# Kernel tuning notes

Hardware: AMD Instinct MI355X
Metric: run time of the kernel (lower is better)

The kernel has to match this reference:

```python
import jax, jax.numpy as jnp
import numpy as np

N_NODES = 20000
N_EDGES = 640000
FEAT = 128


def setup_inputs() -> dict:
    key = jax.random.key(0)
    k1, k2, k3, k4 = jax.random.split(key, 4)
    x = jax.random.normal(k1, (1, N_NODES, FEAT, 4), dtype=jnp.float32)
    edge_index = jax.random.randint(k2, (2, N_EDGES), 0, N_NODES, dtype=jnp.int64)
    # Linear(in_channels=128, out_channels=128): W [out, in], b [out]
    W = jax.random.normal(k3, (FEAT, FEAT), dtype=jnp.float32) * 0.05
    b = jax.random.normal(k4, (FEAT,), dtype=jnp.float32) * 0.05
    return {"x": x, "edge_index": edge_index, "W": W, "b": b}


def reference(x, edge_index, W, b):
    # x: [B, N, F, T]
    B, N, F, T = x.shape
    # permute -> [B, T, N, F]; Linear over feature dim (out == in == F)
    h = jnp.einsum('bnft,of->btno', x, W) + b          # [B, T, N, F]
    h = h.reshape(B * T, N, F)                          # flatten batch*time
    src = edge_index[0]  # message source (x_j)
    dst = edge_index[1]  # scatter target
    msgs = h[:, src, :]                                 # [B*T, E, F] gather
    # scatter-max per target node (PyG aggr='max'); vmap over batch*time
    agg = jax.vmap(lambda m: jax.ops.segment_max(m, dst, num_segments=N))(msgs)
    # nodes with no incoming edges: segment_max yields -inf -> 0 (PyG fill)
    agg = jnp.where(jnp.isneginf(agg), jnp.zeros_like(agg), agg)
    out = agg.reshape(B, T, N, F).transpose(0, 2, 3, 1)  # [B, N, F, T]
    return out
```

## Files before the change

### kernel.cpp

```cpp
#include <hip/hip_runtime.h>
#include <hip/hip_bf16.h>
#include <stdint.h>

#define N_NODES 20000
#define N_EDGES 640000
#define FEAT 128
#define CAPD 128
#define NPHASE 8

typedef __attribute__((ext_vector_type(8))) short bf16x8;
typedef __attribute__((ext_vector_type(4))) float f32x4;

__device__ __forceinline__ unsigned pkbf16(float lo, float hi) {
  __hip_bfloat162 p = __float22bfloat162_rn(make_float2(lo, hi));
  return *reinterpret_cast<unsigned*>(&p);
}

__device__ __forceinline__ unsigned short enc16(float f) {
  unsigned a = __float_as_uint(f);
  unsigned b = (a + 0x7FFFu + ((a >> 16) & 1u)) >> 16;
  unsigned s = (unsigned)((int)a >> 31);
  return (unsigned short)((b ^ 0x8000u) ^ (s & 0x7FFFu));
}

__device__ __forceinline__ float dec16(unsigned e) {
  unsigned b = (e & 0x8000u) ? (e ^ 0x8000u) : (e ^ 0xFFFFu);
  return __uint_as_float(b << 16);
}

__device__ __forceinline__ void pmax(unsigned& a, unsigned v) {
  asm("v_pk_max_u16 %0, %0, %1" : "+v"(a) : "v"(v));
}

#define PMX4(v)                                              \
  do {                                                       \
    pmax(a0, (v).x); pmax(a1, (v).y);                        \
    pmax(a2, (v).z); pmax(a3, (v).w);                        \
  } while (0)

__global__ __launch_bounds__(256) void scatter_kernel(const int* __restrict__ ei,
                                                      int* __restrict__ cnt,
                                                      unsigned short* __restrict__ csr,
                                                      const float* __restrict__ W,
                                                      unsigned short* __restrict__ Wbf) {
  int t = blockIdx.x * 256 + threadIdx.x;
  if (t < FEAT * FEAT / 2) {
    float2 w = ((const float2*)W)[t];
    ((unsigned*)Wbf)[t] = pkbf16(w.x, w.y);
  }
  int src = ei[t];
  int dst = ei[N_EDGES + t];
  int pos = atomicAdd(&cnt[dst], 1);
  if (pos < CAPD) csr[(size_t)dst * CAPD + pos] = (unsigned short)src;
}

__global__ __launch_bounds__(256) void gemm_kernel(
    const float4* __restrict__ x, const unsigned short* __restrict__ Wbf,
    const float* __restrict__ b, uint4* __restrict__ h) {
  __shared__ __align__(16) unsigned short sm[17408 / 2];
  const int tid = threadIdx.x;
  const int n0 = blockIdx.x * 16;

#pragma unroll
  for (int it = 0; it < 4; ++it) {
    int e = tid + it * 256;
    int n = e >> 6, fp = e & 63;
    float4 a = x[(size_t)(n0 + n) * 128 + 2 * fp];
    float4 c = x[(size_t)(n0 + n) * 128 + 2 * fp + 1];
    ((unsigned*)sm)[(0 * 16 + n) * 68 + fp] = pkbf16(a.x, c.x);
    ((unsigned*)sm)[(1 * 16 + n) * 68 + fp] = pkbf16(a.y, c.y);
    ((unsigned*)sm)[(2 * 16 + n) * 68 + fp] = pkbf16(a.z, c.z);
    ((unsigned*)sm)[(3 * 16 + n) * 68 + fp] = pkbf16(a.w, c.w);
  }

  __syncthreads();

  const int wv = tid >> 6;
  const int l = tid & 63;
  const int col = l & 15;
  const int quad = l >> 4;

  f32x4 acc[8];
#pragma unroll
  for (int os = 0; os < 8; ++os) {
    float bv = b[os * 16 + col];
    acc[os] = (f32x4){bv, bv, bv, bv};
  }

#pragma unroll
  for (int k = 0; k < 4; ++k) {
    bf16x8 af = *(const bf16x8*)&sm[(wv * 16 + col) * 136 + k * 32 + quad * 8];
#pragma unroll
    for (int os = 0; os < 8; ++os) {
      bf16x8 bfv = *(const bf16x8*)&Wbf[(os * 16 + col) * 128 + k * 32 + quad * 8];
      acc[os] = __builtin_amdgcn_mfma_f32_16x16x32_bf16(af, bfv, acc[os], 0, 0, 0);
    }
  }

  __syncthreads();

#pragma unroll
  for (int os = 0; os < 8; ++os) {
#pragma unroll
    for (int r = 0; r < 4; ++r) {
      sm[(quad * 4 + r) * 520 + (os * 16 + col) * 4 + wv] = enc16(acc[os][r]);
    }
  }
  __syncthreads();

#pragma unroll
  for (int it = 0; it < 4; ++it) {
    int e = tid + it * 256;
    int n = e >> 6, q = e & 63;
    uint4 v = *(const uint4*)&sm[n * 520 + q * 8];
    h[(size_t)(n0 + n) * 64 + q] = v;
  }
}

__global__ __launch_bounds__(256) void agg_kernel(
    const uint4* __restrict__ h, const int* __restrict__ cnt,
    const unsigned short* __restrict__ csr, float4* __restrict__ out) {
  __shared__ __align__(16) unsigned short sidx[32][136];
  const int bid = blockIdx.x;
  const int p = bid & 7;
  const int grp = bid >> 3;
  const int n0 = grp * 32;
  const int tid = threadIdx.x;

  {
    int r = tid >> 3;
    int q = tid & 7;
    const uint4* srow = (const uint4*)(csr + (size_t)(n0 + r) * CAPD);
    *(uint4*)&sidx[r][q * 8] = srow[q];
    *(uint4*)&sidx[r][(q + 8) * 8] = srow[q + 8];
  }
  __syncthreads();

  const int w = tid >> 6;
  const int lane = tid & 63;
  const int g = lane >> 3;
  const int oq = lane & 7;
  const int n = n0 + w * 8 + g;

  int deg = cnt[n];
  deg = deg > CAPD ? CAPD : deg;

  const unsigned short* myrow = sidx[w * 8 + g];
  int idx0 = (deg > 0) ? (int)myrow[0] : 0;

  int dmax = deg;
#pragma unroll
  for (int d = 8; d <= 32; d <<= 1) {
    int o = __shfl_xor(dmax, d);
    dmax = o > dmax ? o : dmax;
  }
  dmax = __builtin_amdgcn_readfirstlane(dmax);

  unsigned a0 = 0x007F007Fu, a1 = a0, a2 = a0, a3 = a0;
  const char* hb = (const char*)h;
  const unsigned pb = (((unsigned)p * 8 + oq) << 4);

  for (int jb = 0; jb < dmax; jb += 8) {
    uint4 iv = *(const uint4*)&myrow[jb];
    int e0 = (int)(iv.x & 0xFFFFu), e1 = (int)(iv.x >> 16);
    int e2 = (int)(iv.y & 0xFFFFu), e3 = (int)(iv.y >> 16);
    int e4 = (int)(iv.z & 0xFFFFu), e5 = (int)(iv.z >> 16);
    int e6 = (int)(iv.w & 0xFFFFu), e7 = (int)(iv.w >> 16);
    e0 = (jb + 0 < deg) ? e0 : idx0;
    e1 = (jb + 1 < deg) ? e1 : idx0;
    e2 = (jb + 2 < deg) ? e2 : idx0;
    e3 = (jb + 3 < deg) ? e3 : idx0;
    e4 = (jb + 4 < deg) ? e4 : idx0;
    e5 = (jb + 5 < deg) ? e5 : idx0;
    e6 = (jb + 6 < deg) ? e6 : idx0;
    e7 = (jb + 7 < deg) ? e7 : idx0;
    uint4 v0 = *(const uint4*)(hb + (((unsigned)e0 << 10) + pb));
    uint4 v1 = *(const uint4*)(hb + (((unsigned)e1 << 10) + pb));
    uint4 v2 = *(const uint4*)(hb + (((unsigned)e2 << 10) + pb));
    uint4 v3 = *(const uint4*)(hb + (((unsigned)e3 << 10) + pb));
    uint4 v4 = *(const uint4*)(hb + (((unsigned)e4 << 10) + pb));
    uint4 v5 = *(const uint4*)(hb + (((unsigned)e5 << 10) + pb));
    uint4 v6 = *(const uint4*)(hb + (((unsigned)e6 << 10) + pb));
    uint4 v7 = *(const uint4*)(hb + (((unsigned)e7 << 10) + pb));
    PMX4(v0); PMX4(v1); PMX4(v2); PMX4(v3);
    PMX4(v4); PMX4(v5); PMX4(v6); PMX4(v7);
  }

  float4 o0, o1;
  if (deg == 0) {
    o0 = make_float4(0.f, 0.f, 0.f, 0.f);
    o1 = o0;
  } else {
    o0 = make_float4(dec16(a0 & 0xFFFFu), dec16(a0 >> 16),
                     dec16(a1 & 0xFFFFu), dec16(a1 >> 16));
    o1 = make_float4(dec16(a2 & 0xFFFFu), dec16(a2 >> 16),
                     dec16(a3 & 0xFFFFu), dec16(a3 >> 16));
  }
  out[(size_t)n * 128 + p * 16 + oq * 2] = o0;
  out[(size_t)n * 128 + p * 16 + oq * 2 + 1] = o1;
}

extern "C" void kernel_launch(void* const* d_in, const int* in_sizes, int n_in,
                              void* d_out, int out_size, void* d_ws, size_t ws_size,
                              hipStream_t stream) {
  const float* x = (const float*)d_in[0];
  const int* ei = (const int*)d_in[1];
  const float* W = (const float*)d_in[2];
  const float* b = (const float*)d_in[3];
  float* out = (float*)d_out;

  char* ws = (char*)d_ws;
  uint4* h = (uint4*)ws;
  int* cnt = (int*)(ws + 20480000);
  unsigned short* csr = (unsigned short*)(ws + 20560000);
  unsigned short* Wbf = (unsigned short*)(ws + 25680000);

  hipMemsetAsync(cnt, 0, N_NODES * sizeof(int), stream);
  scatter_kernel<<<N_EDGES / 256, 256, 0, stream>>>(ei, cnt, csr, W, Wbf);
  gemm_kernel<<<N_NODES / 16, 256, 0, stream>>>((const float4*)x, Wbf, b, h);
  agg_kernel<<<(N_NODES / 32) * NPHASE, 256, 0, stream>>>(h, cnt, csr, (float4*)out);
}
```

Before: 192.9 us.

## Fuse edge scatter into GEMM kernel, pad counters, double-buffer gather loop

Moves the CSR-building atomic scatter into the GEMM kernel (1250 blocks × 512 edges covers all edges), and replaces the memset plus W conversion with a single init kernel. Per-node counters are spread to a 64-byte stride to reduce atomic contention and false sharing on the same cache line. The aggregation loop is rewritten to double-buffer two batches of 8 gathered rows so loads for the next batch are in flight while the current batch is max-reduced, and launch bounds request 4 waves per SIMD. The trade-off is higher register pressure in the aggregation kernel, a larger zeroing pass (16x the counter memory), and extra work in every GEMM block.

```diff
diff --git a/kernel.cpp b/kernel.cpp
--- a/kernel.cpp
+++ b/kernel.cpp
@@ -7,6 +7,7 @@
 #define FEAT 128
 #define CAPD 128
 #define NPHASE 8
+#define CNTSTRIDE 16
 
 typedef __attribute__((ext_vector_type(8))) short bf16x8;
 typedef __attribute__((ext_vector_type(4))) float f32x4;
@@ -38,28 +39,34 @@
     pmax(a2, (v).z); pmax(a3, (v).w);                        \
   } while (0)
 
-__global__ __launch_bounds__(256) void scatter_kernel(const int* __restrict__ ei,
-                                                      int* __restrict__ cnt,
-                                                      unsigned short* __restrict__ csr,
-                                                      const float* __restrict__ W,
-                                                      unsigned short* __restrict__ Wbf) {
-  int t = blockIdx.x * 256 + threadIdx.x;
-  if (t < FEAT * FEAT / 2) {
-    float2 w = ((const float2*)W)[t];
-    ((unsigned*)Wbf)[t] = pkbf16(w.x, w.y);
-  }
-  int src = ei[t];
-  int dst = ei[N_EDGES + t];
-  int pos = atomicAdd(&cnt[dst], 1);
-  if (pos < CAPD) csr[(size_t)dst * CAPD + pos] = (unsigned short)src;
-}
-
-__global__ __launch_bounds__(256) void gemm_kernel(
+__global__ void init_kernel(const float* __restrict__ W,
+                            unsigned short* __restrict__ Wbf,
+                            int* __restrict__ cnt) {
+  int i = blockIdx.x * 256 + threadIdx.x;
+  if (i < N_NODES * CNTSTRIDE) cnt[i] = 0;
+  if (i < FEAT * FEAT / 2) {
+    float2 w = ((const float2*)W)[i];
+    ((unsigned*)Wbf)[i] = pkbf16(w.x, w.y);
+  }
+}
+
+__global__ __launch_bounds__(256) void gemm_scatter_kernel(
     const float4* __restrict__ x, const unsigned short* __restrict__ Wbf,
-    const float* __restrict__ b, uint4* __restrict__ h) {
+    const float* __restrict__ b, uint4* __restrict__ h,
+    const int* __restrict__ ei, int* __restrict__ cnt,
+    unsigned short* __restrict__ csr) {
   __shared__ __align__(16) unsigned short sm[17408 / 2];
   const int tid = threadIdx.x;
   const int n0 = blockIdx.x * 16;
+
+#pragma unroll
+  for (int r = 0; r < 2; ++r) {
+    int e = blockIdx.x * 512 + r * 256 + tid;
+    int src = ei[e];
+    int dst = ei[N_EDGES + e];
+    int pos = atomicAdd(&cnt[dst * CNTSTRIDE], 1);
+    if (pos < CAPD) csr[(size_t)dst * CAPD + pos] = (unsigned short)src;
+  }
 
 #pragma unroll
   for (int it = 0; it < 4; ++it) {
@@ -117,7 +124,33 @@
   }
 }
 
-__global__ __launch_bounds__(256) void agg_kernel(
+#define CLAMP8(P, ivv, base)                                            \
+  int P##0 = ((base) + 0 < deg) ? (int)((ivv).x & 0xFFFFu) : idx0;      \
+  int P##1 = ((base) + 1 < deg) ? (int)((ivv).x >> 16) : idx0;          \
+  int P##2 = ((base) + 2 < deg) ? (int)((ivv).y & 0xFFFFu) : idx0;      \
+  int P##3 = ((base) + 3 < deg) ? (int)((ivv).y >> 16) : idx0;          \
+  int P##4 = ((base) + 4 < deg) ? (int)((ivv).z & 0xFFFFu) : idx0;      \
+  int P##5 = ((base) + 5 < deg) ? (int)((ivv).z >> 16) : idx0;          \
+  int P##6 = ((base) + 6 < deg) ? (int)((ivv).w & 0xFFFFu) : idx0;      \
+  int P##7 = ((base) + 7 < deg) ? (int)((ivv).w >> 16) : idx0;
+
+#define ISSUE8(V, P)                                                    \
+  V##0 = *(const uint4*)(hb + (((unsigned)P##0 << 10) + pb));           \
+  V##1 = *(const uint4*)(hb + (((unsigned)P##1 << 10) + pb));           \
+  V##2 = *(const uint4*)(hb + (((unsigned)P##2 << 10) + pb));           \
+  V##3 = *(const uint4*)(hb + (((unsigned)P##3 << 10) + pb));           \
+  V##4 = *(const uint4*)(hb + (((unsigned)P##4 << 10) + pb));           \
+  V##5 = *(const uint4*)(hb + (((unsigned)P##5 << 10) + pb));           \
+  V##6 = *(const uint4*)(hb + (((unsigned)P##6 << 10) + pb));           \
+  V##7 = *(const uint4*)(hb + (((unsigned)P##7 << 10) + pb));
+
+#define PMAX8(V)                                                        \
+  do {                                                                  \
+    PMX4(V##0); PMX4(V##1); PMX4(V##2); PMX4(V##3);                     \
+    PMX4(V##4); PMX4(V##5); PMX4(V##6); PMX4(V##7);                     \
+  } while (0)
+
+__global__ __launch_bounds__(256, 4) void agg_kernel(
     const uint4* __restrict__ h, const int* __restrict__ cnt,
     const unsigned short* __restrict__ csr, float4* __restrict__ out) {
   __shared__ __align__(16) unsigned short sidx[32][136];
@@ -142,7 +175,7 @@
   const int oq = lane & 7;
   const int n = n0 + w * 8 + g;
 
-  int deg = cnt[n];
+  int deg = cnt[n * CNTSTRIDE];
   deg = deg > CAPD ? CAPD : deg;
 
   const unsigned short* myrow = sidx[w * 8 + g];
@@ -160,30 +193,35 @@
   const char* hb = (const char*)h;
   const unsigned pb = (((unsigned)p * 8 + oq) << 4);
 
-  for (int jb = 0; jb < dmax; jb += 8) {
-    uint4 iv = *(const uint4*)&myrow[jb];
-    int e0 = (int)(iv.x & 0xFFFFu), e1 = (int)(iv.x >> 16);
-    int e2 = (int)(iv.y & 0xFFFFu), e3 = (int)(iv.y >> 16);
-    int e4 = (int)(iv.z & 0xFFFFu), e5 = (int)(iv.z >> 16);
-    int e6 = (int)(iv.w & 0xFFFFu), e7 = (int)(iv.w >> 16);
-    e0 = (jb + 0 < deg) ? e0 : idx0;
-    e1 = (jb + 1 < deg) ? e1 : idx0;
-    e2 = (jb + 2 < deg) ? e2 : idx0;
-    e3 = (jb + 3 < deg) ? e3 : idx0;
-    e4 = (jb + 4 < deg) ? e4 : idx0;
-    e5 = (jb + 5 < deg) ? e5 : idx0;
-    e6 = (jb + 6 < deg) ? e6 : idx0;
-    e7 = (jb + 7 < deg) ? e7 : idx0;
-    uint4 v0 = *(const uint4*)(hb + (((unsigned)e0 << 10) + pb));
-    uint4 v1 = *(const uint4*)(hb + (((unsigned)e1 << 10) + pb));
-    uint4 v2 = *(const uint4*)(hb + (((unsigned)e2 << 10) + pb));
-    uint4 v3 = *(const uint4*)(hb + (((unsigned)e3 << 10) + pb));
-    uint4 v4 = *(const uint4*)(hb + (((unsigned)e4 << 10) + pb));
-    uint4 v5 = *(const uint4*)(hb + (((unsigned)e5 << 10) + pb));
-    uint4 v6 = *(const uint4*)(hb + (((unsigned)e6 << 10) + pb));
-    uint4 v7 = *(const uint4*)(hb + (((unsigned)e7 << 10) + pb));
-    PMX4(v0); PMX4(v1); PMX4(v2); PMX4(v3);
-    PMX4(v4); PMX4(v5); PMX4(v6); PMX4(v7);
+  if (dmax > 0) {
+    const int dmax16 = (dmax + 15) & ~15;
+    uint4 vA0, vA1, vA2, vA3, vA4, vA5, vA6, vA7;
+    uint4 vB0, vB1, vB2, vB3, vB4, vB5, vB6, vB7;
+    {
+      uint4 iv = *(const uint4*)&myrow[0];
+      CLAMP8(eA, iv, 0);
+      ISSUE8(vA, eA);
+    }
+    int jb = 0;
+    while (true) {
+      {
+        uint4 iv = *(const uint4*)&myrow[jb + 8];
+        CLAMP8(eB, iv, jb + 8);
+        ISSUE8(vB, eB);
+      }
+      PMAX8(vA);
+      jb += 16;
+      if (jb >= dmax16) {
+        PMAX8(vB);
+        break;
+      }
+      {
+        uint4 iv = *(const uint4*)&myrow[jb];
+        CLAMP8(eA2, iv, jb);
+        ISSUE8(vA, eA2);
+      }
+      PMAX8(vB);
+    }
   }
 
   float4 o0, o1;
@@ -212,11 +250,11 @@
   char* ws = (char*)d_ws;
   uint4* h = (uint4*)ws;
   int* cnt = (int*)(ws + 20480000);
-  unsigned short* csr = (unsigned short*)(ws + 20560000);
-  unsigned short* Wbf = (unsigned short*)(ws + 25680000);
-
-  hipMemsetAsync(cnt, 0, N_NODES * sizeof(int), stream);
-  scatter_kernel<<<N_EDGES / 256, 256, 0, stream>>>(ei, cnt, csr, W, Wbf);
-  gemm_kernel<<<N_NODES / 16, 256, 0, stream>>>((const float4*)x, Wbf, b, h);
+  unsigned short* csr = (unsigned short*)(ws + 21760000);
+  unsigned short* Wbf = (unsigned short*)(ws + 26880000);
+
+  init_kernel<<<(N_NODES * CNTSTRIDE + 255) / 256, 256, 0, stream>>>(W, Wbf, cnt);
+  gemm_scatter_kernel<<<N_NODES / 16, 256, 0, stream>>>((const float4*)x, Wbf, b, h,
+                                                        ei, cnt, csr);
   agg_kernel<<<(N_NODES / 32) * NPHASE, 256, 0, stream>>>(h, cnt, csr, (float4*)out);
 }
```

Result: no change. 195.8 us (+1.5%).

## Fuse edge scatter into GEMM kernel and pad degree counters

Applied to the files above, without the earlier changes.

The edge-bucketing scatter moves into the GEMM kernel, which now uses 512 threads per block: every thread handles one edge while waves 0-3 run the MFMA GEMM. The memset and the W conversion become a single init kernel, and the per-node counters are padded to a 16-int stride to spread atomic contention across cache lines. The aim is to cut one launch, let scatter atomics overlap the x loads and GEMM, and reduce atomic line contention. In exchange the counter array grows 16x and must be zeroed by a kernel, and half the waves sit idle during the GEMM.

```diff
diff --git a/kernel.cpp b/kernel.cpp
--- a/kernel.cpp
+++ b/kernel.cpp
@@ -7,6 +7,7 @@
 #define FEAT 128
 #define CAPD 128
 #define NPHASE 8
+#define CNTSTRIDE 16
 
 typedef __attribute__((ext_vector_type(8))) short bf16x8;
 typedef __attribute__((ext_vector_type(4))) float f32x4;
@@ -38,40 +39,50 @@
     pmax(a2, (v).z); pmax(a3, (v).w);                        \
   } while (0)
 
-__global__ __launch_bounds__(256) void scatter_kernel(const int* __restrict__ ei,
-                                                      int* __restrict__ cnt,
-                                                      unsigned short* __restrict__ csr,
-                                                      const float* __restrict__ W,
-                                                      unsigned short* __restrict__ Wbf) {
-  int t = blockIdx.x * 256 + threadIdx.x;
-  if (t < FEAT * FEAT / 2) {
-    float2 w = ((const float2*)W)[t];
-    ((unsigned*)Wbf)[t] = pkbf16(w.x, w.y);
-  }
-  int src = ei[t];
-  int dst = ei[N_EDGES + t];
-  int pos = atomicAdd(&cnt[dst], 1);
-  if (pos < CAPD) csr[(size_t)dst * CAPD + pos] = (unsigned short)src;
-}
-
-__global__ __launch_bounds__(256) void gemm_kernel(
+__global__ void init_kernel(const float* __restrict__ W,
+                            unsigned short* __restrict__ Wbf,
+                            int* __restrict__ cnt) {
+  int i = blockIdx.x * 256 + threadIdx.x;
+  if (i < N_NODES * CNTSTRIDE) cnt[i] = 0;
+  if (i < FEAT * FEAT / 2) {
+    float2 w = ((const float2*)W)[i];
+    ((unsigned*)Wbf)[i] = pkbf16(w.x, w.y);
+  }
+}
+
+__global__ __launch_bounds__(512) void gemm_scatter_kernel(
     const float4* __restrict__ x, const unsigned short* __restrict__ Wbf,
-    const float* __restrict__ b, uint4* __restrict__ h) {
+    const float* __restrict__ b, uint4* __restrict__ h,
+    const int* __restrict__ ei, int* __restrict__ cnt,
+    unsigned short* __restrict__ csr) {
   __shared__ __align__(16) unsigned short sm[17408 / 2];
   const int tid = threadIdx.x;
   const int n0 = blockIdx.x * 16;
 
-#pragma unroll
-  for (int it = 0; it < 4; ++it) {
-    int e = tid + it * 256;
-    int n = e >> 6, fp = e & 63;
-    float4 a = x[(size_t)(n0 + n) * 128 + 2 * fp];
-    float4 c = x[(size_t)(n0 + n) * 128 + 2 * fp + 1];
-    ((unsigned*)sm)[(0 * 16 + n) * 68 + fp] = pkbf16(a.x, c.x);
-    ((unsigned*)sm)[(1 * 16 + n) * 68 + fp] = pkbf16(a.y, c.y);
-    ((unsigned*)sm)[(2 * 16 + n) * 68 + fp] = pkbf16(a.z, c.z);
-    ((unsigned*)sm)[(3 * 16 + n) * 68 + fp] = pkbf16(a.w, c.w);
-  }
+  const int eid = blockIdx.x * 512 + tid;
+  int src = ei[eid];
+  int dst = ei[N_EDGES + eid];
+
+  const int e0 = tid, e1 = tid + 512;
+  const int na = e0 >> 6, fa = e0 & 63;
+  const int nb = e1 >> 6, fb = e1 & 63;
+  float4 a0 = x[(size_t)(n0 + na) * 128 + 2 * fa];
+  float4 c0 = x[(size_t)(n0 + na) * 128 + 2 * fa + 1];
+  float4 a1 = x[(size_t)(n0 + nb) * 128 + 2 * fb];
+  float4 c1 = x[(size_t)(n0 + nb) * 128 + 2 * fb + 1];
+
+  int pos = atomicAdd(&cnt[dst * CNTSTRIDE], 1);
+
+  ((unsigned*)sm)[(0 * 16 + na) * 68 + fa] = pkbf16(a0.x, c0.x);
+  ((unsigned*)sm)[(1 * 16 + na) * 68 + fa] = pkbf16(a0.y, c0.y);
+  ((unsigned*)sm)[(2 * 16 + na) * 68 + fa] = pkbf16(a0.z, c0.z);
+  ((unsigned*)sm)[(3 * 16 + na) * 68 + fa] = pkbf16(a0.w, c0.w);
+  ((unsigned*)sm)[(0 * 16 + nb) * 68 + fb] = pkbf16(a1.x, c1.x);
+  ((unsigned*)sm)[(1 * 16 + nb) * 68 + fb] = pkbf16(a1.y, c1.y);
+  ((unsigned*)sm)[(2 * 16 + nb) * 68 + fb] = pkbf16(a1.z, c1.z);
+  ((unsigned*)sm)[(3 * 16 + nb) * 68 + fb] = pkbf16(a1.w, c1.w);
+
+  if (pos < CAPD) csr[(size_t)dst * CAPD + pos] = (unsigned short)src;
 
   __syncthreads();
 
@@ -80,37 +91,41 @@
   const int col = l & 15;
   const int quad = l >> 4;
 
-  f32x4 acc[8];
-#pragma unroll
-  for (int os = 0; os < 8; ++os) {
-    float bv = b[os * 16 + col];
-    acc[os] = (f32x4){bv, bv, bv, bv};
-  }
-
-#pragma unroll
-  for (int k = 0; k < 4; ++k) {
-    bf16x8 af = *(const bf16x8*)&sm[(wv * 16 + col) * 136 + k * 32 + quad * 8];
+  if (wv < 4) {
+    f32x4 acc[8];
 #pragma unroll
     for (int os = 0; os < 8; ++os) {
-      bf16x8 bfv = *(const bf16x8*)&Wbf[(os * 16 + col) * 128 + k * 32 + quad * 8];
-      acc[os] = __builtin_amdgcn_mfma_f32_16x16x32_bf16(af, bfv, acc[os], 0, 0, 0);
+      float bv = b[os * 16 + col];
+      acc[os] = (f32x4){bv, bv, bv, bv};
     }
-  }
-
+
+#pragma unroll
+    for (int k = 0; k < 4; ++k) {
+      bf16x8 af = *(const bf16x8*)&sm[(wv * 16 + col) * 136 + k * 32 + quad * 8];
+#pragma unroll
+      for (int os = 0; os < 8; ++os) {
+        bf16x8 bfv = *(const bf16x8*)&Wbf[(os * 16 + col) * 128 + k * 32 + quad * 8];
+        acc[os] = __builtin_amdgcn_mfma_f32_16x16x32_bf16(af, bfv, acc[os], 0, 0, 0);
+      }
+    }
+
+    __syncthreads();
+
+#pragma unroll
+    for (int os = 0; os < 8; ++os) {
+#pragma unroll
+      for (int r = 0; r < 4; ++r) {
+        sm[(quad * 4 + r) * 520 + (os * 16 + col) * 4 + wv] = enc16(acc[os][r]);
+      }
+    }
+  } else {
+    __syncthreads();
+  }
   __syncthreads();
 
 #pragma unroll
-  for (int os = 0; os < 8; ++os) {
-#pragma unroll
-    for (int r = 0; r < 4; ++r) {
-      sm[(quad * 4 + r) * 520 + (os * 16 + col) * 4 + wv] = enc16(acc[os][r]);
-    }
-  }
-  __syncthreads();
-
-#pragma unroll
-  for (int it = 0; it < 4; ++it) {
-    int e = tid + it * 256;
+  for (int it = 0; it < 2; ++it) {
+    int e = tid + it * 512;
     int n = e >> 6, q = e & 63;
     uint4 v = *(const uint4*)&sm[n * 520 + q * 8];
     h[(size_t)(n0 + n) * 64 + q] = v;
@@ -142,7 +157,7 @@
   const int oq = lane & 7;
   const int n = n0 + w * 8 + g;
 
-  int deg = cnt[n];
+  int deg = cnt[n * CNTSTRIDE];
   deg = deg > CAPD ? CAPD : deg;
 
   const unsigned short* myrow = sidx[w * 8 + g];
@@ -212,11 +227,11 @@
   char* ws = (char*)d_ws;
   uint4* h = (uint4*)ws;
   int* cnt = (int*)(ws + 20480000);
-  unsigned short* csr = (unsigned short*)(ws + 20560000);
-  unsigned short* Wbf = (unsigned short*)(ws + 25680000);
-
-  hipMemsetAsync(cnt, 0, N_NODES * sizeof(int), stream);
-  scatter_kernel<<<N_EDGES / 256, 256, 0, stream>>>(ei, cnt, csr, W, Wbf);
-  gemm_kernel<<<N_NODES / 16, 256, 0, stream>>>((const float4*)x, Wbf, b, h);
+  unsigned short* csr = (unsigned short*)(ws + 21760000);
+  unsigned short* Wbf = (unsigned short*)(ws + 26880000);
+
+  init_kernel<<<(N_NODES * CNTSTRIDE + 255) / 256, 256, 0, stream>>>(W, Wbf, cnt);
+  gemm_scatter_kernel<<<N_NODES / 16, 512, 0, stream>>>((const float4*)x, Wbf, b, h,
+                                                        ei, cnt, csr);
   agg_kernel<<<(N_NODES / 32) * NPHASE, 256, 0, stream>>>(h, cnt, csr, (float4*)out);
 }
```

Measured after the change: 180.6 us. -6.4%, faster.
